# Kernel optimization log

Hardware: AMD Instinct MI355X
Metric: run time of the kernel (lower is better)

## Reference

```python
import jax, jax.numpy as jnp
import numpy as np

INF = jnp.float32(jnp.inf)
# 8 grid directions (the torch module always uses all 8; self.diagonal is never read)
DIRS = jnp.array([[-1, 0], [1, 0], [0, -1], [0, 1],
                  [-1, -1], [-1, 1], [1, -1], [1, 1]], dtype=jnp.int32)


def setup_inputs() -> dict:
    key = jax.random.key(0)
    b, n = 128, 32
    weights = jax.random.uniform(key, (b, n, n), dtype=jnp.float32)
    return {"weights": weights}


def _dijkstra_path(weights):
    b, n, _ = weights.shape
    ar = jnp.arange(b)

    dist = jnp.full((b, n, n), INF, dtype=weights.dtype).at[:, 0, 0].set(0.0)
    vis = jnp.zeros((b, n, n), dtype=bool)
    pred = jnp.zeros((b, n, n, 2), dtype=jnp.int32)

    def relax_step(_, state):
        dist, vis, pred = state
        # pick unvisited node with minimum distance, per batch element
        unvis = jnp.where(vis, INF, dist)                       # (b, n, n)
        idx = jnp.argmin(unvis.reshape(b, -1), axis=1)          # (b,)
        cy, cx = idx // n, idx % n
        vis = vis.at[ar, cy, cx].set(True)
        cur = dist[ar, cy, cx]                                   # (b,)

        # 8 neighbors, vectorized over the direction axis
        ny = cy[:, None] + DIRS[None, :, 0]                      # (b, 8)
        nx = cx[:, None] + DIRS[None, :, 1]
        valid = (ny >= 0) & (ny < n) & (nx >= 0) & (nx < n)
        nyc = jnp.clip(ny, 0, n - 1)
        nxc = jnp.clip(nx, 0, n - 1)
        bb = jnp.broadcast_to(ar[:, None], (b, 8))

        old = dist[bb, nyc, nxc]
        nvis = vis[bb, nyc, nxc]
        new = cur[:, None] + weights[bb, nyc, nxc]
        upd = valid & ~nvis & (new < old)

        # duplicate-safe relaxation: scatter-min with inf where no update
        dist = dist.at[bb, nyc, nxc].min(jnp.where(upd, new, INF))
        # cells updated this step all get predecessor (cy, cx)
        umask = jnp.zeros((b, n, n), dtype=bool).at[bb, nyc, nxc].max(upd)
        cur_yx = jnp.stack([cy, cx], axis=-1)[:, None, None, :]  # (b,1,1,2)
        pred = jnp.where(umask[..., None], cur_yx.astype(pred.dtype), pred)
        return dist, vis, pred

    # Running the full n*n relaxations is equivalent to the torch early-break:
    # by Dijkstra's invariant, the target's distance/predecessor are final once
    # it would be popped, and later pops never alter the target path.
    dist, vis, pred = jax.lax.fori_loop(0, n * n, relax_step, (dist, vis, pred))

    # backtrack from (n-1, n-1) to (0, 0); pred[0,0] == (0,0) so it is a fixed point
    path = jnp.zeros((b, n, n), dtype=jnp.float32).at[:, n - 1, n - 1].set(1.0)

    def back_step(_, state):
        path, cy, cx = state
        py = pred[ar, cy, cx, 0]
        px = pred[ar, cy, cx, 1]
        path = path.at[ar, py, px].set(1.0)
        return path, py, px

    start = jnp.full((b,), n - 1, dtype=jnp.int32)
    path, _, _ = jax.lax.fori_loop(0, n * n, back_step, (path, start, start))
    return path


def reference(weights) -> jnp.ndarray:
    return _dijkstra_path(weights)
```

## Files before the change

kernel.cpp:

```cpp
#include <hip/hip_runtime.h>

#define N   32
#define NN  1024

__global__ __launch_bounds__(64, 1) void dijkstra_path_kernel(
    const float* __restrict__ weights, float* __restrict__ out)
{
    const int b    = blockIdx.x;
    const int lane = threadIdx.x & 63;
    const int ty   = lane >> 3;
    const int tx   = lane & 7;
    const int y0   = ty << 2;
    const int x0   = tx << 2;

    __shared__ int   pred[NN];
    __shared__ float pathf[NN];

    const float INF = __builtin_huge_valf();

    #pragma unroll
    for (int k = 0; k < 16; ++k) pathf[lane + k * 64] = 0.0f;

    float w[4][4];
    const float* wb = weights + b * NN;
    #pragma unroll
    for (int i = 0; i < 4; ++i) {
        const float4 v = *(const float4*)(wb + (y0 + i) * N + x0);
        w[i][0] = v.x; w[i][1] = v.y; w[i][2] = v.z; w[i][3] = v.w;
    }

    float g[6][6];
    #pragma unroll
    for (int i = 0; i < 6; ++i)
        #pragma unroll
        for (int j = 0; j < 6; ++j) g[i][j] = INF;
    if (lane == 0) g[1][1] = 0.0f;

    const bool hT = (ty > 0), hB = (ty < 7), hL = (tx > 0), hR = (tx < 7);

#define EXCHANGE()                                                            \
    {                                                                         \
        float tT[4], tB[4], tL[4], tR[4];                                     \
        _Pragma("unroll")                                                     \
        for (int j = 0; j < 4; ++j) tT[j] = __shfl(g[4][1 + j], lane - 8);    \
        _Pragma("unroll")                                                     \
        for (int j = 0; j < 4; ++j) tB[j] = __shfl(g[1][1 + j], lane + 8);    \
        _Pragma("unroll")                                                     \
        for (int i = 0; i < 4; ++i) tL[i] = __shfl(g[1 + i][4], lane - 1);    \
        _Pragma("unroll")                                                     \
        for (int i = 0; i < 4; ++i) tR[i] = __shfl(g[1 + i][1], lane + 1);    \
        const float cTL = __shfl(g[4][4], lane - 9);                          \
        const float cTR = __shfl(g[4][1], lane - 7);                          \
        const float cBL = __shfl(g[1][4], lane + 7);                          \
        const float cBR = __shfl(g[1][1], lane + 9);                          \
        _Pragma("unroll")                                                     \
        for (int j = 0; j < 4; ++j) {                                         \
            g[0][1 + j] = hT ? tT[j] : INF;                                   \
            g[5][1 + j] = hB ? tB[j] : INF;                                   \
        }                                                                     \
        _Pragma("unroll")                                                     \
        for (int i = 0; i < 4; ++i) {                                         \
            g[1 + i][0] = hL ? tL[i] : INF;                                   \
            g[1 + i][5] = hR ? tR[i] : INF;                                   \
        }                                                                     \
        g[0][0] = (hT && hL) ? cTL : INF;                                     \
        g[0][5] = (hT && hR) ? cTR : INF;                                     \
        g[5][0] = (hB && hL) ? cBL : INF;                                     \
        g[5][5] = (hB && hR) ? cBR : INF;                                     \
    }

#define RELAX(i, j)                                                           \
    {                                                                         \
        const float old = g[(i)][(j)];                                        \
        const float a = fminf(fminf(g[(i)-1][(j)-1], g[(i)-1][(j)]),          \
                              g[(i)-1][(j)+1]);                               \
        const float c = fminf(fminf(g[(i)][(j)-1], g[(i)][(j)+1]),            \
                              g[(i)+1][(j)-1]);                               \
        const float e = fminf(g[(i)+1][(j)], g[(i)+1][(j)+1]);                \
        const float m = fminf(fminf(a, c), e);                                \
        const float nv = m + w[(i)-1][(j)-1];                                 \
        changed |= (nv < old);                                                \
        g[(i)][(j)] = fminf(old, nv);                                         \
    }

    for (int it = 0; it < 768; ++it) {
        bool changed = false;
        EXCHANGE()
        const int d = it & 3;
        if (d == 0) {
            #pragma unroll
            for (int i = 1; i <= 4; ++i)
                #pragma unroll
                for (int j = 1; j <= 4; ++j) RELAX(i, j)
        } else if (d == 1) {
            #pragma unroll
            for (int i = 4; i >= 1; --i)
                #pragma unroll
                for (int j = 1; j <= 4; ++j) RELAX(i, j)
        } else if (d == 2) {
            #pragma unroll
            for (int i = 4; i >= 1; --i)
                #pragma unroll
                for (int j = 4; j >= 1; --j) RELAX(i, j)
        } else {
            #pragma unroll
            for (int i = 1; i <= 4; ++i)
                #pragma unroll
                for (int j = 4; j >= 1; --j) RELAX(i, j)
        }
        if (!__any((int)changed)) break;
    }
#undef RELAX

    EXCHANGE()
#undef EXCHANGE

    const int dy[8] = {-1, 1, 0, 0, -1, -1, 1, 1};
    const int dx[8] = { 0, 0,-1, 1, -1,  1,-1, 1};
    #pragma unroll
    for (int i = 0; i < 4; ++i)
        #pragma unroll
        for (int j = 0; j < 4; ++j) {
            const int yy = y0 + i, xx = x0 + j;
            const int t  = yy * N + xx;
            int p = 0;
            if (t != 0) {
                float best = INF;
                #pragma unroll
                for (int k = 0; k < 8; ++k) {
                    const float u = g[1 + i + dy[k]][1 + j + dx[k]];
                    const float c = u + w[i][j];
                    if (c < best) { best = c; p = (yy + dy[k]) * N + (xx + dx[k]); }
                }
            }
            pred[t] = p;
        }
    __threadfence_block();

    if (lane == 0) {
        int cur = NN - 1;
        pathf[cur] = 1.0f;
        for (int s = 0; s < NN && cur != 0; ++s) {
            cur = pred[cur];
            pathf[cur] = 1.0f;
        }
    }
    __threadfence_block();

    float* ob = out + b * NN;
    #pragma unroll
    for (int i = 0; i < 4; ++i) {
        const int t = (y0 + i) * N + x0;
        const float4 v = *(const float4*)&pathf[t];
        *(float4*)(ob + t) = v;
    }
}

extern "C" void kernel_launch(void* const* d_in, const int* in_sizes, int n_in,
                              void* d_out, int out_size, void* d_ws, size_t ws_size,
                              hipStream_t stream) {
    const float* w = (const float*)d_in[0];
    float* out = (float*)d_out;
    const int b = in_sizes[0] / NN;
    dijkstra_path_kernel<<<dim3(b), dim3(64), 0, stream>>>(w, out);
}
```

Measured before the change: 74.42 us.

## Parallelize path backtrack with pointer jumping and use DPP for lateral exchange

```diff
diff --git a/kernel.cpp b/kernel.cpp
--- a/kernel.cpp
+++ b/kernel.cpp
@@ -2,6 +2,20 @@
 
 #define N   32
 #define NN  1024
+
+
+__device__ __forceinline__ float dpp_from_left(float x) {
+    int r = __builtin_amdgcn_update_dpp(__builtin_bit_cast(int, x),
+                                        __builtin_bit_cast(int, x),
+                                        0x111 , 0xF, 0xF, false);
+    return __builtin_bit_cast(float, r);
+}
+__device__ __forceinline__ float dpp_from_right(float x) {
+    int r = __builtin_amdgcn_update_dpp(__builtin_bit_cast(int, x),
+                                        __builtin_bit_cast(int, x),
+                                        0x101 , 0xF, 0xF, false);
+    return __builtin_bit_cast(float, r);
+}
 
 __global__ __launch_bounds__(64, 1) void dijkstra_path_kernel(
     const float* __restrict__ weights, float* __restrict__ out)
@@ -13,7 +27,7 @@
     const int y0   = ty << 2;
     const int x0   = tx << 2;
 
-    __shared__ int   pred[NN];
+    __shared__ int   anc[7][NN];
     __shared__ float pathf[NN];
 
     const float INF = __builtin_huge_valf();
@@ -40,28 +54,28 @@
 
 #define EXCHANGE()                                                            \
     {                                                                         \
-        float tT[4], tB[4], tL[4], tR[4];                                     \
-        _Pragma("unroll")                                                     \
-        for (int j = 0; j < 4; ++j) tT[j] = __shfl(g[4][1 + j], lane - 8);    \
-        _Pragma("unroll")                                                     \
-        for (int j = 0; j < 4; ++j) tB[j] = __shfl(g[1][1 + j], lane + 8);    \
-        _Pragma("unroll")                                                     \
-        for (int i = 0; i < 4; ++i) tL[i] = __shfl(g[1 + i][4], lane - 1);    \
-        _Pragma("unroll")                                                     \
-        for (int i = 0; i < 4; ++i) tR[i] = __shfl(g[1 + i][1], lane + 1);    \
-        const float cTL = __shfl(g[4][4], lane - 9);                          \
-        const float cTR = __shfl(g[4][1], lane - 7);                          \
-        const float cBL = __shfl(g[1][4], lane + 7);                          \
-        const float cBR = __shfl(g[1][1], lane + 9);                          \
+        float rT[4], rB[4], rL[4], rR[4];                                     \
+        _Pragma("unroll")                                                     \
+        for (int j = 0; j < 4; ++j) rT[j] = __shfl(g[4][1 + j], lane - 8);    \
+        _Pragma("unroll")                                                     \
+        for (int j = 0; j < 4; ++j) rB[j] = __shfl(g[1][1 + j], lane + 8);    \
+        _Pragma("unroll")                                                     \
+        for (int i = 0; i < 4; ++i) rL[i] = dpp_from_left (g[1 + i][4]);      \
+        _Pragma("unroll")                                                     \
+        for (int i = 0; i < 4; ++i) rR[i] = dpp_from_right(g[1 + i][1]);      \
+        const float cTL = dpp_from_left (rT[3]);        \
+        const float cTR = dpp_from_right(rT[0]);        \
+        const float cBL = dpp_from_left (rB[3]);        \
+        const float cBR = dpp_from_right(rB[0]);        \
         _Pragma("unroll")                                                     \
         for (int j = 0; j < 4; ++j) {                                         \
-            g[0][1 + j] = hT ? tT[j] : INF;                                   \
-            g[5][1 + j] = hB ? tB[j] : INF;                                   \
+            g[0][1 + j] = hT ? rT[j] : INF;                                   \
+            g[5][1 + j] = hB ? rB[j] : INF;                                   \
         }                                                                     \
         _Pragma("unroll")                                                     \
         for (int i = 0; i < 4; ++i) {                                         \
-            g[1 + i][0] = hL ? tL[i] : INF;                                   \
-            g[1 + i][5] = hR ? tR[i] : INF;                                   \
+            g[1 + i][0] = hL ? rL[i] : INF;                                   \
+            g[1 + i][5] = hR ? rR[i] : INF;                                   \
         }                                                                     \
         g[0][0] = (hT && hL) ? cTL : INF;                                     \
         g[0][5] = (hT && hR) ? cTR : INF;                                     \
@@ -133,16 +147,48 @@
                     if (c < best) { best = c; p = (yy + dy[k]) * N + (xx + dx[k]); }
                 }
             }
-            pred[t] = p;
+            anc[0][t] = p;
         }
     __threadfence_block();
 
-    if (lane == 0) {
-        int cur = NN - 1;
-        pathf[cur] = 1.0f;
-        for (int s = 0; s < NN && cur != 0; ++s) {
-            cur = pred[cur];
-            pathf[cur] = 1.0f;
+    #pragma unroll
+    for (int k = 1; k < 7; ++k) {
+        int v[16];
+        #pragma unroll
+        for (int c = 0; c < 16; ++c) {
+            const int t = lane + c * 64;
+            v[c] = anc[k - 1][anc[k - 1][t]];
+        }
+        __threadfence_block();
+        #pragma unroll
+        for (int c = 0; c < 16; ++c) anc[k][lane + c * 64] = v[c];
+        __threadfence_block();
+    }
+
+    {
+        int c = NN - 1;
+        #pragma unroll
+        for (int k = 5; k >= 0; --k)
+            if ((lane >> k) & 1) c = anc[k][c];
+        pathf[c] = 1.0f;
+
+        int c64 = anc[6][NN - 1];
+        int c2 = c64;
+        #pragma unroll
+        for (int k = 5; k >= 0; --k)
+            if ((lane >> k) & 1) c2 = anc[k][c2];
+        pathf[c2] = 1.0f;
+
+        if (lane == 0) {
+            int c128 = anc[6][c64];
+            if (c128 != 0) {
+                int cur = c128;
+                for (int s = 0; s < NN && cur != 0; ++s) {
+                    pathf[cur] = 1.0f;
+                    cur = anc[0][cur];
+                }
+                pathf[0] = 1.0f;
+            }
         }
     }
     __threadfence_block();
```

New measurement: 72.51 us. 2.6% less time.
